# Kernel tuning notes

Hardware: AMD Instinct MI355X
Metric: run time of the kernel (lower is better)

## Reference

```python
import jax, jax.numpy as jnp
import numpy as np

B, N, D, H = 8, 1024, 1024, 16
DH = D // H
EPS = 1e-5


def setup_inputs() -> dict:
    key = jax.random.key(0)
    ks = jax.random.split(key, 12)
    s = 0.02
    return {
        "k": jax.random.normal(ks[0], (B, N, D), jnp.float32),
        "q": jax.random.normal(ks[1], (B, N, D), jnp.float32),
        "r": jax.random.normal(ks[2], (B, N, D), jnp.float32),
        "Wk": jax.random.normal(ks[3], (D, D), jnp.float32) * s,
        "bk": jnp.zeros((D,), jnp.float32),
        "Wq": jax.random.normal(ks[4], (D, D), jnp.float32) * s,
        "bq": jnp.zeros((D,), jnp.float32),
        "Wv": jax.random.normal(ks[5], (D, D), jnp.float32) * s,
        "bv": jnp.zeros((D,), jnp.float32),
        "Wo": jax.random.normal(ks[6], (D, D), jnp.float32) * s,
        "bo": jnp.zeros((D,), jnp.float32),
        "g1": jnp.ones((D,), jnp.float32),
        "b1": jnp.zeros((D,), jnp.float32),
        "g2": jnp.ones((D,), jnp.float32),
        "b2": jnp.zeros((D,), jnp.float32),
    }


def _layer_norm(x, g, b):
    mu = jnp.mean(x, axis=-1, keepdims=True)
    var = jnp.mean(jnp.square(x - mu), axis=-1, keepdims=True)
    return (x - mu) * jax.lax.rsqrt(var + EPS) * g + b


def reference(k, q, r, Wk, bk, Wq, bq, Wv, bv, Wo, bo, g1, b1, g2, b2):
    # linear projections (torch Linear: x @ W.T + b)
    kh = (k @ Wk.T + bk).reshape(B, -1, H, DH).transpose(0, 2, 1, 3)  # [B,H,Nk,DH]
    qh = (q @ Wq.T + bq).reshape(B, -1, H, DH).transpose(0, 2, 1, 3)  # [B,H,Nq,DH]
    vh = (r @ Wv.T + bv).reshape(B, -1, H, DH).transpose(0, 2, 1, 3)  # [B,H,Nk,DH]
    scale = 1.0 / jnp.sqrt(jnp.float32(DH))
    scores = jnp.einsum('bhid,bhjd->bhij', qh, kh) * scale  # [B,H,Nq,Nk]
    attn = jax.nn.softmax(scores, axis=-1)
    o = jnp.einsum('bhij,bhjd->bhid', attn, vh)  # [B,H,Nq,DH]
    o = o.transpose(0, 2, 1, 3).reshape(B, -1, D)
    mha = o @ Wo.T + bo
    residual = _layer_norm(mha + q, g1, b1)
    # source bug: mlp = nn.ReLU(BatchLinear(...)) -> mlp is plain ReLU
    out = _layer_norm(jax.nn.relu(residual) + residual, g2, b2)
    return out
```

## Files before the change

### kernel.cpp

```cpp
#include <hip/hip_runtime.h>
#include <hip/hip_bf16.h>
#include <math.h>

#define BB 8
#define NN 1024
#define DD 1024
#define HH 16
#define DH 64
#define MTOK 8192

typedef __attribute__((ext_vector_type(8))) short short8;
typedef __attribute__((ext_vector_type(4))) short short4v;
typedef __attribute__((ext_vector_type(4))) float float4v;

__device__ __forceinline__ ushort f2bf(float f) {
    union { float f; unsigned u; } v; v.f = f;
    unsigned r = v.u + 0x7fffu + ((v.u >> 16) & 1u);
    return (ushort)(r >> 16);
}

__device__ __forceinline__ void gl_lds16(const ushort* g, ushort* l) {
    __builtin_amdgcn_global_load_lds(
        (const __attribute__((address_space(1))) void*)g,
        (__attribute__((address_space(3))) void*)l, 16, 0, 0);
}

__device__ __forceinline__ void stage8f(const float* __restrict__ p, ushort* d) {
    float4v a = *(const float4v*)p;
    float4v b = *(const float4v*)(p + 4);
    short8 s;
    s[0]=(short)f2bf(a[0]); s[1]=(short)f2bf(a[1]); s[2]=(short)f2bf(a[2]); s[3]=(short)f2bf(a[3]);
    s[4]=(short)f2bf(b[0]); s[5]=(short)f2bf(b[1]); s[6]=(short)f2bf(b[2]); s[7]=(short)f2bf(b[3]);
    *(short8*)d = s;
}

struct CvtArgs {
    const float* src[7];
    ushort* dst[7];
    int n[7];
};
__global__ __launch_bounds__(256) void cvt_bf16(CvtArgs a) {
    const int z = blockIdx.y;
    const int idx = (blockIdx.x * 256 + threadIdx.x) * 8;
    if (idx >= a.n[z]) return;
    const float* s = a.src[z];
    float4v x0 = *(const float4v*)(s + idx);
    float4v x1 = *(const float4v*)(s + idx + 4);
    short8 o;
    o[0]=(short)f2bf(x0[0]); o[1]=(short)f2bf(x0[1]); o[2]=(short)f2bf(x0[2]); o[3]=(short)f2bf(x0[3]);
    o[4]=(short)f2bf(x1[0]); o[5]=(short)f2bf(x1[1]); o[6]=(short)f2bf(x1[2]); o[7]=(short)f2bf(x1[3]);
    *(short8*)(a.dst[z] + idx) = o;
}

template <typename TA, typename TW, int MODE>
__device__ __forceinline__ void gemm_core(const void* Ap, const void* Wp,
                                          const float* __restrict__ bias,
                                          void* __restrict__ outp,
                                          ushort* As, ushort* Bs) {
    constexpr bool A_BF = (sizeof(TA) == 2);
    constexpr bool W_BF = (sizeof(TW) == 2);
    constexpr int LDA = A_BF ? 64 : 72;
    constexpr int LDB = W_BF ? 64 : 72;

    const int tid  = threadIdx.x;
    const int wid  = tid >> 6;
    const int lane = tid & 63;
    const int quad = lane >> 4;
    const int l15  = lane & 15;
    const int wr   = wid >> 1;
    const int wc   = wid & 1;
    const int m0   = blockIdx.y * 128;
    const int n0   = blockIdx.x * 128;

    float4v acc[4][4] = {};

    for (int kt = 0; kt < 16; ++kt) {
        const int k0 = kt * 64;
        if constexpr (A_BF) {
            const ushort* A = (const ushort*)Ap;
            for (int t = 0; t < 4; ++t) {
                int chunk = t * 4 + wid;
                int row   = chunk * 8 + (lane >> 3);
                int kc    = (lane & 7) * 8;
                gl_lds16(A + (size_t)(m0 + row) * 1024 + k0 + kc, As + chunk * 512);
            }
        } else {
            const float* A = (const float*)Ap;
            for (int i = 0; i < 4; ++i) {
                int cidx = i * 256 + tid;
                int row  = cidx >> 3;
                int kc   = (cidx & 7) * 8;
                stage8f(A + (size_t)(m0 + row) * 1024 + k0 + kc, &As[row * 72 + kc]);
            }
        }
        if constexpr (W_BF) {
            const ushort* W = (const ushort*)Wp;
            for (int t = 0; t < 4; ++t) {
                int chunk = t * 4 + wid;
                int row   = chunk * 8 + (lane >> 3);
                int kc    = (lane & 7) * 8;
                gl_lds16(W + (size_t)(n0 + row) * 1024 + k0 + kc, Bs + chunk * 512);
            }
        } else {
            const float* W = (const float*)Wp;
            for (int i = 0; i < 4; ++i) {
                int cidx = i * 256 + tid;
                int row  = cidx >> 3;
                int kc   = (cidx & 7) * 8;
                stage8f(W + (size_t)(n0 + row) * 1024 + k0 + kc, &Bs[row * 72 + kc]);
            }
        }
        __syncthreads();

        for (int kk = 0; kk < 2; ++kk) {
            const int ko = kk * 32 + quad * 8;
            short8 af[4], bfr[4];
            for (int i = 0; i < 4; ++i)
                af[i] = *(const short8*)&As[(wr * 64 + i * 16 + l15) * LDA + ko];
            for (int j = 0; j < 4; ++j)
                bfr[j] = *(const short8*)&Bs[(wc * 64 + j * 16 + l15) * LDB + ko];
            for (int i = 0; i < 4; ++i)
                for (int j = 0; j < 4; ++j)
                    acc[i][j] = __builtin_amdgcn_mfma_f32_16x16x32_bf16(af[i], bfr[j], acc[i][j], 0, 0, 0);
        }
        __syncthreads();
    }

    for (int j = 0; j < 4; ++j) {
        const int col = n0 + wc * 64 + j * 16 + l15;
        const float bv = bias[col];
        const int h = col >> 6;
        const int d = col & 63;
        for (int i = 0; i < 4; ++i) {
            const int rowbase = m0 + wr * 64 + i * 16 + quad * 4;
            if constexpr (MODE == 0) {
                ushort* out = (ushort*)outp;
                for (int r = 0; r < 4; ++r) {
                    int row = rowbase + r;
                    int bi = row >> 10, n = row & 1023;
                    out[(((size_t)(bi * HH + h) * NN + n) * DH) + d] =
                        f2bf(acc[i][j][r] + bv);
                }
            } else if constexpr (MODE == 1) {
                ushort* out = (ushort*)outp;
                int bi = rowbase >> 10, n = rowbase & 1023;
                short4v pk;
                for (int r = 0; r < 4; ++r) pk[r] = (short)f2bf(acc[i][j][r] + bv);
                *(short4v*)&out[(((size_t)(bi * HH + h) * DH + d) * NN) + n] = pk;
            } else {
                float* out = (float*)outp;
                for (int r = 0; r < 4; ++r)
                    out[(size_t)(rowbase + r) * 1024 + col] = acc[i][j][r] + bv;
            }
        }
    }
}

template <typename TA, typename TW>
__global__ __launch_bounds__(256) void proj3(const void* q, const void* k, const void* r,
                                             const void* Wq, const void* Wk, const void* Wv,
                                             const float* bq, const float* bk, const float* bv,
                                             ushort* qh, ushort* kh, ushort* vt) {
    __shared__ ushort As[128 * 72];
    __shared__ ushort Bs[128 * 72];
    if (blockIdx.z == 0)      gemm_core<TA, TW, 0>(q, Wq, bq, qh, As, Bs);
    else if (blockIdx.z == 1) gemm_core<TA, TW, 0>(k, Wk, bk, kh, As, Bs);
    else                      gemm_core<TA, TW, 1>(r, Wv, bv, vt, As, Bs);
}

template <typename TA, typename TW>
__global__ __launch_bounds__(256) void gemm_out(const void* A, const void* W,
                                                const float* bias, float* out) {
    __shared__ ushort As[128 * 72];
    __shared__ ushort Bs[128 * 72];
    gemm_core<TA, TW, 2>(A, W, bias, out, As, Bs);
}

__global__ __launch_bounds__(256) void attn_fused(const ushort* __restrict__ qh,
                                                  const ushort* __restrict__ kh,
                                                  const ushort* __restrict__ vt,
                                                  ushort* __restrict__ o) {
    __shared__ ushort Ks[64 * 64];
    __shared__ ushort Vs[64 * 64];
    __shared__ ushort Ps[4][16 * 72];

    const int tid  = threadIdx.x;
    const int wid  = tid >> 6;
    const int lane = tid & 63;
    const int quad = lane >> 4;
    const int l15  = lane & 15;
    const int qt   = blockIdx.x;
    const int h    = blockIdx.y;
    const int b    = blockIdx.z;

    const ushort* qb = qh + (size_t)(b * HH + h) * NN * DH;
    const ushort* kb = kh + (size_t)(b * HH + h) * NN * DH;
    const ushort* vb = vt + (size_t)(b * HH + h) * DH * NN;

    const int qrow = qt * 64 + wid * 16 + l15;
    short8 qf[2];
    qf[0] = *(const short8*)(qb + (size_t)qrow * DH + quad * 8);
    qf[1] = *(const short8*)(qb + (size_t)qrow * DH + 32 + quad * 8);

    float lsum[4] = {0.f, 0.f, 0.f, 0.f};
    float4v oacc[4] = {};
    ushort* Pw = Ps[wid];
    const float SCL = 0.18033688011f;

    for (int kt = 0; kt < 16; ++kt) {
        for (int t = 0; t < 2; ++t) {
            int chunk = t * 4 + wid;
            int row   = chunk * 8 + (lane >> 3);
            int kc    = (lane & 7) * 8;
            gl_lds16(kb + (size_t)(kt * 64 + row) * DH + kc, Ks + chunk * 512);
            gl_lds16(vb + (size_t)row * NN + kt * 64 + kc, Vs + chunk * 512);
        }
        __syncthreads();

        float4v sacc[4] = {};
        for (int c = 0; c < 4; ++c)
            for (int s = 0; s < 2; ++s) {
                short8 kf = *(const short8*)&Ks[(c * 16 + l15) * 64 + s * 32 + quad * 8];
                sacc[c] = __builtin_amdgcn_mfma_f32_16x16x32_bf16(qf[s], kf, sacc[c], 0, 0, 0);
            }

        for (int c = 0; c < 4; ++c)
            for (int r = 0; r < 4; ++r) {
                float p = exp2f(sacc[c][r] * SCL);
                lsum[r] += p;
                Pw[(quad * 4 + r) * 72 + c * 16 + l15] = f2bf(p);
            }

        for (int s = 0; s < 2; ++s) {
            short8 pf = *(const short8*)&Pw[l15 * 72 + s * 32 + quad * 8];
            for (int nn = 0; nn < 4; ++nn) {
                short8 vf = *(const short8*)&Vs[(nn * 16 + l15) * 64 + s * 32 + quad * 8];
                oacc[nn] = __builtin_amdgcn_mfma_f32_16x16x32_bf16(pf, vf, oacc[nn], 0, 0, 0);
            }
        }
        __syncthreads();
    }

    for (int r = 0; r < 4; ++r) {
        float t = lsum[r];
        t += __shfl_xor(t, 1);
        t += __shfl_xor(t, 2);
        t += __shfl_xor(t, 4);
        t += __shfl_xor(t, 8);
        float inv = 1.0f / t;
        int row = qt * 64 + wid * 16 + quad * 4 + r;
        size_t base = ((size_t)b * NN + row) * DD + h * 64;
        for (int nn = 0; nn < 4; ++nn)
            o[base + nn * 16 + l15] = f2bf(oacc[nn][r] * inv);
    }
}

__global__ __launch_bounds__(256) void ln_fuse(const float* __restrict__ mha,
                                               const float* __restrict__ q,
                                               const float* __restrict__ g1,
                                               const float* __restrict__ b1,
                                               const float* __restrict__ g2,
                                               const float* __restrict__ b2,
                                               float* __restrict__ out) {
    __shared__ float red1[8];
    __shared__ float red2[8];
    const int tid  = threadIdx.x;
    const int wid  = tid >> 6;
    const int lane = tid & 63;
    const size_t base = (size_t)blockIdx.x * 1024 + tid * 4;

    float4v xv = *(const float4v*)(mha + base);
    float4v qv = *(const float4v*)(q + base);
    float x[4];
    float s = 0.f, ss = 0.f;
    for (int i = 0; i < 4; ++i) {
        x[i] = xv[i] + qv[i];
        s += x[i]; ss += x[i] * x[i];
    }
    for (int off = 1; off < 64; off <<= 1) {
        s += __shfl_xor(s, off); ss += __shfl_xor(ss, off);
    }
    if (lane == 0) { red1[wid * 2] = s; red1[wid * 2 + 1] = ss; }
    __syncthreads();
    s  = red1[0] + red1[2] + red1[4] + red1[6];
    ss = red1[1] + red1[3] + red1[5] + red1[7];
    float mu = s * (1.0f / 1024.0f);
    float rstd = rsqrtf(ss * (1.0f / 1024.0f) - mu * mu + 1e-5f);

    float4v g1v = *(const float4v*)(g1 + tid * 4);
    float4v b1v = *(const float4v*)(b1 + tid * 4);
    float y[4];
    float s2 = 0.f, ss2 = 0.f;
    for (int i = 0; i < 4; ++i) {
        float rr = (x[i] - mu) * rstd * g1v[i] + b1v[i];
        y[i] = fmaxf(rr, 0.f) + rr;
        s2 += y[i]; ss2 += y[i] * y[i];
    }
    for (int off = 1; off < 64; off <<= 1) {
        s2 += __shfl_xor(s2, off); ss2 += __shfl_xor(ss2, off);
    }
    if (lane == 0) { red2[wid * 2] = s2; red2[wid * 2 + 1] = ss2; }
    __syncthreads();
    s2  = red2[0] + red2[2] + red2[4] + red2[6];
    ss2 = red2[1] + red2[3] + red2[5] + red2[7];
    float mu2 = s2 * (1.0f / 1024.0f);
    float rstd2 = rsqrtf(ss2 * (1.0f / 1024.0f) - mu2 * mu2 + 1e-5f);

    float4v g2v = *(const float4v*)(g2 + tid * 4);
    float4v b2v = *(const float4v*)(b2 + tid * 4);
    float4v ov;
    for (int i = 0; i < 4; ++i) ov[i] = (y[i] - mu2) * rstd2 * g2v[i] + b2v[i];
    *(float4v*)(out + base) = ov;
}

extern "C" void kernel_launch(void* const* d_in, const int* in_sizes, int n_in,
                              void* d_out, int out_size, void* d_ws, size_t ws_size,
                              hipStream_t stream) {
    const float* k  = (const float*)d_in[0];
    const float* q  = (const float*)d_in[1];
    const float* r  = (const float*)d_in[2];
    const float* Wk = (const float*)d_in[3];
    const float* bk = (const float*)d_in[4];
    const float* Wq = (const float*)d_in[5];
    const float* bq = (const float*)d_in[6];
    const float* Wv = (const float*)d_in[7];
    const float* bv = (const float*)d_in[8];
    const float* Wo = (const float*)d_in[9];
    const float* bo = (const float*)d_in[10];
    const float* g1 = (const float*)d_in[11];
    const float* b1 = (const float*)d_in[12];
    const float* g2 = (const float*)d_in[13];
    const float* b2 = (const float*)d_in[14];

    char* ws = (char*)d_ws;
    const size_t MB = 1u << 20;
    dim3 blk(256);

    if (ws_size >= 121 * MB) {
        ushort* qc  = (ushort*)(ws);
        ushort* kc  = (ushort*)(ws + 16 * MB);
        ushort* rc  = (ushort*)(ws + 32 * MB);
        ushort* Wqc = (ushort*)(ws + 48 * MB);
        ushort* Wkc = (ushort*)(ws + 50 * MB);
        ushort* Wvc = (ushort*)(ws + 52 * MB);
        ushort* Woc = (ushort*)(ws + 54 * MB);
        ushort* qh  = (ushort*)(ws + 56 * MB);
        ushort* kh  = (ushort*)(ws + 72 * MB);
        ushort* vt  = (ushort*)(ws + 88 * MB);
        ushort* ob  = (ushort*)(ws + 104 * MB);
        float*  mh  = (float*)(ws);

        CvtArgs ca;
        ca.src[0] = q;  ca.dst[0] = qc;  ca.n[0] = MTOK * DD;
        ca.src[1] = k;  ca.dst[1] = kc;  ca.n[1] = MTOK * DD;
        ca.src[2] = r;  ca.dst[2] = rc;  ca.n[2] = MTOK * DD;
        ca.src[3] = Wq; ca.dst[3] = Wqc; ca.n[3] = DD * DD;
        ca.src[4] = Wk; ca.dst[4] = Wkc; ca.n[4] = DD * DD;
        ca.src[5] = Wv; ca.dst[5] = Wvc; ca.n[5] = DD * DD;
        ca.src[6] = Wo; ca.dst[6] = Woc; ca.n[6] = DD * DD;
        cvt_bf16<<<dim3(4096, 7), blk, 0, stream>>>(ca);

        proj3<ushort, ushort><<<dim3(8, 64, 3), blk, 0, stream>>>(
            qc, kc, rc, Wqc, Wkc, Wvc, bq, bk, bv, qh, kh, vt);
        attn_fused<<<dim3(16, HH, BB), blk, 0, stream>>>(qh, kh, vt, ob);
        gemm_out<ushort, ushort><<<dim3(8, 64), blk, 0, stream>>>(ob, Woc, bo, mh);
        ln_fuse<<<dim3(MTOK), blk, 0, stream>>>(mh, q, g1, b1, g2, b2, (float*)d_out);
    } else {
        ushort* qh  = (ushort*)(ws);
        ushort* kh  = (ushort*)(ws + 16 * MB);
        ushort* vt  = (ushort*)(ws + 32 * MB);
        ushort* ob  = (ushort*)(ws + 48 * MB);
        ushort* Wqc = (ushort*)(ws + 48 * MB);
        ushort* Wkc = (ushort*)(ws + 50 * MB);
        ushort* Wvc = (ushort*)(ws + 52 * MB);
        float*  mh  = (float*)(ws);

        CvtArgs ca;
        ca.src[0] = Wq; ca.dst[0] = Wqc; ca.n[0] = DD * DD;
        ca.src[1] = Wk; ca.dst[1] = Wkc; ca.n[1] = DD * DD;
        ca.src[2] = Wv; ca.dst[2] = Wvc; ca.n[2] = DD * DD;
        for (int i = 3; i < 7; ++i) { ca.src[i] = Wq; ca.dst[i] = Wqc; ca.n[i] = 0; }
        cvt_bf16<<<dim3(512, 3), blk, 0, stream>>>(ca);

        proj3<float, ushort><<<dim3(8, 64, 3), blk, 0, stream>>>(
            q, k, r, Wqc, Wkc, Wvc, bq, bk, bv, qh, kh, vt);
        attn_fused<<<dim3(16, HH, BB), blk, 0, stream>>>(qh, kh, vt, ob);
        gemm_out<ushort, float><<<dim3(8, 64), blk, 0, stream>>>(ob, Wo, bo, mh);
        ln_fuse<<<dim3(MTOK), blk, 0, stream>>>(mh, q, g1, b1, g2, b2, (float*)d_out);
    }
}
```

Baseline: 386.1 us.

## Swizzle LDS tiles, transpose MFMA operands for vector stores, double query rows per attention wave

The bf16 GEMM and attention tiles now use an XOR-swizzled LDS layout, meant to remove bank conflicts on the short8 fragment reads. In the GEMMs, modes 0 and 2 swap the MFMA operand order so each lane holds four consecutive output features, which allows vectorized short4/float4 stores and a vector bias load. The attention kernel now processes 128 query rows per block, with each wave handling two 16-row groups. This reuses each K and V fragment across two MFMAs and halves K/V reloads, at the cost of more registers and a smaller grid reordered with batch-head first. The P tile is written transposed with vector stores and the row-sum reduction changes to match.

Result: faster. 363.3 us (-5.9%).

```diff
diff --git a/kernel.cpp b/kernel.cpp
--- a/kernel.cpp
+++ b/kernel.cpp
@@ -71,6 +71,7 @@
     const int wc   = wid & 1;
     const int m0   = blockIdx.y * 128;
     const int n0   = blockIdx.x * 128;
+    const int sw   = l15 & 7;
 
     float4v acc[4][4] = {};
 
@@ -78,14 +79,16 @@
         const int k0 = kt * 64;
         if constexpr (A_BF) {
             const ushort* A = (const ushort*)Ap;
+            #pragma unroll
             for (int t = 0; t < 4; ++t) {
                 int chunk = t * 4 + wid;
                 int row   = chunk * 8 + (lane >> 3);
-                int kc    = (lane & 7) * 8;
+                int kc    = ((lane & 7) ^ (lane >> 3)) * 8;
                 gl_lds16(A + (size_t)(m0 + row) * 1024 + k0 + kc, As + chunk * 512);
             }
         } else {
             const float* A = (const float*)Ap;
+            #pragma unroll
             for (int i = 0; i < 4; ++i) {
                 int cidx = i * 256 + tid;
                 int row  = cidx >> 3;
@@ -95,14 +98,16 @@
         }
         if constexpr (W_BF) {
             const ushort* W = (const ushort*)Wp;
+            #pragma unroll
             for (int t = 0; t < 4; ++t) {
                 int chunk = t * 4 + wid;
                 int row   = chunk * 8 + (lane >> 3);
-                int kc    = (lane & 7) * 8;
+                int kc    = ((lane & 7) ^ (lane >> 3)) * 8;
                 gl_lds16(W + (size_t)(n0 + row) * 1024 + k0 + kc, Bs + chunk * 512);
             }
         } else {
             const float* W = (const float*)Wp;
+            #pragma unroll
             for (int i = 0; i < 4; ++i) {
                 int cidx = i * 256 + tid;
                 int row  = cidx >> 3;
@@ -112,45 +117,72 @@
         }
         __syncthreads();
 
+        #pragma unroll
         for (int kk = 0; kk < 2; ++kk) {
-            const int ko = kk * 32 + quad * 8;
             short8 af[4], bfr[4];
+            #pragma unroll
             for (int i = 0; i < 4; ++i)
-                af[i] = *(const short8*)&As[(wr * 64 + i * 16 + l15) * LDA + ko];
+                af[i] = *(const short8*)&As[(wr * 64 + i * 16 + l15) * LDA +
+                        (A_BF ? (((kk * 4 + quad) ^ sw) * 8) : (kk * 32 + quad * 8))];
+            #pragma unroll
             for (int j = 0; j < 4; ++j)
-                bfr[j] = *(const short8*)&Bs[(wc * 64 + j * 16 + l15) * LDB + ko];
+                bfr[j] = *(const short8*)&Bs[(wc * 64 + j * 16 + l15) * LDB +
+                         (W_BF ? (((kk * 4 + quad) ^ sw) * 8) : (kk * 32 + quad * 8))];
+            #pragma unroll
             for (int i = 0; i < 4; ++i)
-                for (int j = 0; j < 4; ++j)
-                    acc[i][j] = __builtin_amdgcn_mfma_f32_16x16x32_bf16(af[i], bfr[j], acc[i][j], 0, 0, 0);
+                #pragma unroll
+                for (int j = 0; j < 4; ++j) {
+                    if constexpr (MODE == 1)
+                        acc[i][j] = __builtin_amdgcn_mfma_f32_16x16x32_bf16(af[i], bfr[j], acc[i][j], 0, 0, 0);
+                    else
+                        acc[j][i] = __builtin_amdgcn_mfma_f32_16x16x32_bf16(bfr[j], af[i], acc[j][i], 0, 0, 0);
+                }
         }
         __syncthreads();
     }
 
-    for (int j = 0; j < 4; ++j) {
-        const int col = n0 + wc * 64 + j * 16 + l15;
-        const float bv = bias[col];
-        const int h = col >> 6;
-        const int d = col & 63;
-        for (int i = 0; i < 4; ++i) {
-            const int rowbase = m0 + wr * 64 + i * 16 + quad * 4;
-            if constexpr (MODE == 0) {
-                ushort* out = (ushort*)outp;
-                for (int r = 0; r < 4; ++r) {
-                    int row = rowbase + r;
-                    int bi = row >> 10, n = row & 1023;
-                    out[(((size_t)(bi * HH + h) * NN + n) * DH) + d] =
-                        f2bf(acc[i][j][r] + bv);
-                }
-            } else if constexpr (MODE == 1) {
-                ushort* out = (ushort*)outp;
+    if constexpr (MODE == 1) {
+        ushort* out = (ushort*)outp;
+        #pragma unroll
+        for (int j = 0; j < 4; ++j) {
+            const int col = n0 + wc * 64 + j * 16 + l15;
+            const float bv = bias[col];
+            const int h = col >> 6;
+            const int d = col & 63;
+            #pragma unroll
+            for (int i = 0; i < 4; ++i) {
+                const int rowbase = m0 + wr * 64 + i * 16 + quad * 4;
                 int bi = rowbase >> 10, n = rowbase & 1023;
                 short4v pk;
+                #pragma unroll
                 for (int r = 0; r < 4; ++r) pk[r] = (short)f2bf(acc[i][j][r] + bv);
                 *(short4v*)&out[(((size_t)(bi * HH + h) * DH + d) * NN) + n] = pk;
-            } else {
-                float* out = (float*)outp;
-                for (int r = 0; r < 4; ++r)
-                    out[(size_t)(rowbase + r) * 1024 + col] = acc[i][j][r] + bv;
+            }
+        }
+    } else {
+        #pragma unroll
+        for (int p = 0; p < 4; ++p) {
+            const int fb = n0 + wc * 64 + p * 16 + quad * 4;
+            const float4v bv4 = *(const float4v*)&bias[fb];
+            const int h = fb >> 6;
+            const int d = fb & 63;
+            #pragma unroll
+            for (int q = 0; q < 4; ++q) {
+                const int tok = m0 + wr * 64 + q * 16 + l15;
+                if constexpr (MODE == 0) {
+                    ushort* out = (ushort*)outp;
+                    int bi = tok >> 10, n = tok & 1023;
+                    short4v pk;
+                    #pragma unroll
+                    for (int r = 0; r < 4; ++r) pk[r] = (short)f2bf(acc[p][q][r] + bv4[r]);
+                    *(short4v*)&out[(((size_t)(bi * HH + h) * NN + n) * DH) + d] = pk;
+                } else {
+                    float* out = (float*)outp;
+                    float4v ov;
+                    #pragma unroll
+                    for (int r = 0; r < 4; ++r) ov[r] = acc[p][q][r] + bv4[r];
+                    *(float4v*)&out[(size_t)tok * 1024 + fb] = ov;
+                }
             }
         }
     }
@@ -182,76 +214,103 @@
                                                   ushort* __restrict__ o) {
     __shared__ ushort Ks[64 * 64];
     __shared__ ushort Vs[64 * 64];
-    __shared__ ushort Ps[4][16 * 72];
+    __shared__ ushort Ps[4][2][16 * 72];
 
     const int tid  = threadIdx.x;
     const int wid  = tid >> 6;
     const int lane = tid & 63;
     const int quad = lane >> 4;
     const int l15  = lane & 15;
-    const int qt   = blockIdx.x;
-    const int h    = blockIdx.y;
-    const int b    = blockIdx.z;
-
-    const ushort* qb = qh + (size_t)(b * HH + h) * NN * DH;
-    const ushort* kb = kh + (size_t)(b * HH + h) * NN * DH;
-    const ushort* vb = vt + (size_t)(b * HH + h) * DH * NN;
-
-    const int qrow = qt * 64 + wid * 16 + l15;
-    short8 qf[2];
-    qf[0] = *(const short8*)(qb + (size_t)qrow * DH + quad * 8);
-    qf[1] = *(const short8*)(qb + (size_t)qrow * DH + 32 + quad * 8);
-
-    float lsum[4] = {0.f, 0.f, 0.f, 0.f};
-    float4v oacc[4] = {};
-    ushort* Pw = Ps[wid];
+    const int sw   = l15 & 7;
+    const int bh   = blockIdx.x;
+    const int qt   = blockIdx.y;
+    const int h    = bh & 15;
+    const int b    = bh >> 4;
+
+    const ushort* qb = qh + (size_t)bh * NN * DH;
+    const ushort* kb = kh + (size_t)bh * NN * DH;
+    const ushort* vb = vt + (size_t)bh * DH * NN;
+
+    short8 qf[2][2];
+    #pragma unroll
+    for (int u = 0; u < 2; ++u) {
+        const int qrow = qt * 128 + wid * 32 + u * 16 + l15;
+        qf[u][0] = *(const short8*)(qb + (size_t)qrow * DH + quad * 8);
+        qf[u][1] = *(const short8*)(qb + (size_t)qrow * DH + 32 + quad * 8);
+    }
+
+    float lsum[2] = {0.f, 0.f};
+    float4v oaccT[2][4] = {};
     const float SCL = 0.18033688011f;
 
     for (int kt = 0; kt < 16; ++kt) {
+        #pragma unroll
         for (int t = 0; t < 2; ++t) {
             int chunk = t * 4 + wid;
             int row   = chunk * 8 + (lane >> 3);
-            int kc    = (lane & 7) * 8;
+            int kc    = ((lane & 7) ^ (lane >> 3)) * 8;
             gl_lds16(kb + (size_t)(kt * 64 + row) * DH + kc, Ks + chunk * 512);
             gl_lds16(vb + (size_t)row * NN + kt * 64 + kc, Vs + chunk * 512);
         }
         __syncthreads();
 
-        float4v sacc[4] = {};
-        for (int c = 0; c < 4; ++c)
-            for (int s = 0; s < 2; ++s) {
-                short8 kf = *(const short8*)&Ks[(c * 16 + l15) * 64 + s * 32 + quad * 8];
-                sacc[c] = __builtin_amdgcn_mfma_f32_16x16x32_bf16(qf[s], kf, sacc[c], 0, 0, 0);
-            }
-
-        for (int c = 0; c < 4; ++c)
-            for (int r = 0; r < 4; ++r) {
-                float p = exp2f(sacc[c][r] * SCL);
-                lsum[r] += p;
-                Pw[(quad * 4 + r) * 72 + c * 16 + l15] = f2bf(p);
-            }
-
+        float4v sacc[2][4] = {};
+        #pragma unroll
+        for (int s = 0; s < 2; ++s)
+            #pragma unroll
+            for (int c = 0; c < 4; ++c) {
+                short8 kf = *(const short8*)&Ks[(c * 16 + l15) * 64 + ((s * 4 + quad) ^ sw) * 8];
+                #pragma unroll
+                for (int u = 0; u < 2; ++u)
+                    sacc[u][c] = __builtin_amdgcn_mfma_f32_16x16x32_bf16(kf, qf[u][s], sacc[u][c], 0, 0, 0);
+            }
+
+        #pragma unroll
+        for (int u = 0; u < 2; ++u)
+            #pragma unroll
+            for (int c = 0; c < 4; ++c) {
+                short4v pk;
+                #pragma unroll
+                for (int rr = 0; rr < 4; ++rr) {
+                    float p = exp2f(sacc[u][c][rr] * SCL);
+                    lsum[u] += p;
+                    pk[rr] = (short)f2bf(p);
+                }
+                *(short4v*)&Ps[wid][u][l15 * 72 + c * 16 + quad * 4] = pk;
+            }
+
+        #pragma unroll
         for (int s = 0; s < 2; ++s) {
-            short8 pf = *(const short8*)&Pw[l15 * 72 + s * 32 + quad * 8];
+            short8 pf[2];
+            #pragma unroll
+            for (int u = 0; u < 2; ++u)
+                pf[u] = *(const short8*)&Ps[wid][u][l15 * 72 + s * 32 + quad * 8];
+            #pragma unroll
             for (int nn = 0; nn < 4; ++nn) {
-                short8 vf = *(const short8*)&Vs[(nn * 16 + l15) * 64 + s * 32 + quad * 8];
-                oacc[nn] = __builtin_amdgcn_mfma_f32_16x16x32_bf16(pf, vf, oacc[nn], 0, 0, 0);
+                short8 vf = *(const short8*)&Vs[(nn * 16 + l15) * 64 + ((s * 4 + quad) ^ sw) * 8];
+                #pragma unroll
+                for (int u = 0; u < 2; ++u)
+                    oaccT[u][nn] = __builtin_amdgcn_mfma_f32_16x16x32_bf16(vf, pf[u], oaccT[u][nn], 0, 0, 0);
             }
         }
         __syncthreads();
     }
 
-    for (int r = 0; r < 4; ++r) {
-        float t = lsum[r];
-        t += __shfl_xor(t, 1);
-        t += __shfl_xor(t, 2);
-        t += __shfl_xor(t, 4);
-        t += __shfl_xor(t, 8);
+    #pragma unroll
+    for (int u = 0; u < 2; ++u) {
+        float t = lsum[u];
+        t += __shfl_xor(t, 16);
+        t += __shfl_xor(t, 32);
         float inv = 1.0f / t;
-        int row = qt * 64 + wid * 16 + quad * 4 + r;
-        size_t base = ((size_t)b * NN + row) * DD + h * 64;
-        for (int nn = 0; nn < 4; ++nn)
-            o[base + nn * 16 + l15] = f2bf(oacc[nn][r] * inv);
+        int row = qt * 128 + wid * 32 + u * 16 + l15;
+        size_t base = ((size_t)b * NN + row) * DD + h * 64 + quad * 4;
+        #pragma unroll
+        for (int nn = 0; nn < 4; ++nn) {
+            short4v pk;
+            #pragma unroll
+            for (int rr = 0; rr < 4; ++rr) pk[rr] = (short)f2bf(oaccT[u][nn][rr] * inv);
+            *(short4v*)&o[base + nn * 16] = pk;
+        }
     }
 }
 
@@ -362,7 +421,7 @@
 
         proj3<ushort, ushort><<<dim3(8, 64, 3), blk, 0, stream>>>(
             qc, kc, rc, Wqc, Wkc, Wvc, bq, bk, bv, qh, kh, vt);
-        attn_fused<<<dim3(16, HH, BB), blk, 0, stream>>>(qh, kh, vt, ob);
+        attn_fused<<<dim3(HH * BB, 8), blk, 0, stream>>>(qh, kh, vt, ob);
         gemm_out<ushort, ushort><<<dim3(8, 64), blk, 0, stream>>>(ob, Woc, bo, mh);
         ln_fuse<<<dim3(MTOK), blk, 0, stream>>>(mh, q, g1, b1, g2, b2, (float*)d_out);
     } else {
@@ -384,7 +443,7 @@
 
         proj3<float, ushort><<<dim3(8, 64, 3), blk, 0, stream>>>(
             q, k, r, Wqc, Wkc, Wvc, bq, bk, bv, qh, kh, vt);
-        attn_fused<<<dim3(16, HH, BB), blk, 0, stream>>>(qh, kh, vt, ob);
+        attn_fused<<<dim3(HH * BB, 8), blk, 0, stream>>>(qh, kh, vt, ob);
         gemm_out<ushort, float><<<dim3(8, 64), blk, 0, stream>>>(ob, Wo, bo, mh);
         ln_fuse<<<dim3(MTOK), blk, 0, stream>>>(mh, q, g1, b1, g2, b2, (float*)d_out);
     }
```
